# Kernel optimization log

Measured on AMD Instinct MI355X. Metric: run time of the kernel, lower is better.

The kernel has to match this reference:

```python
import jax, jax.numpy as jnp
import numpy as np

B, S, H, R = 32, 512, 1024, 64


def _bernoulli(key, shape, p=0.05):
    return (jax.random.uniform(key, shape) < p).astype(jnp.float32)


def setup_inputs() -> dict:
    key = jax.random.key(0)
    ks = jax.random.split(key, 16)
    context = jax.random.normal(ks[0], (B, S, H), dtype=jnp.float32)
    masks = jnp.ones((B, S), dtype=jnp.float32)
    all_subject_heads = _bernoulli(ks[1], (B, S))
    all_subject_tails = _bernoulli(ks[2], (B, S))
    # one-hot subject head/tail positions (tail >= head)
    h_pos = jax.random.randint(ks[3], (B,), 0, S // 2)
    t_pos = h_pos + jax.random.randint(ks[4], (B,), 0, 8)
    subject_head = jax.nn.one_hot(h_pos, S, dtype=jnp.float32)
    subject_tail = jax.nn.one_hot(t_pos, S, dtype=jnp.float32)
    object_heads = _bernoulli(ks[5], (B, S, R))
    object_tails = _bernoulli(ks[6], (B, S, R))
    # learned parameters (PyTorch Linear: y = x @ W.T + b; store as [in, out])
    sc = 1.0 / np.sqrt(H)
    Ws_h = jax.random.uniform(ks[7], (H, 1), minval=-sc, maxval=sc)
    bs_h = jnp.zeros((1,), dtype=jnp.float32)
    Ws_t = jax.random.uniform(ks[8], (H, 1), minval=-sc, maxval=sc)
    bs_t = jnp.zeros((1,), dtype=jnp.float32)
    Wo_h = jax.random.uniform(ks[9], (H, R), minval=-sc, maxval=sc)
    bo_h = jnp.zeros((R,), dtype=jnp.float32)
    Wo_t = jax.random.uniform(ks[10], (H, R), minval=-sc, maxval=sc)
    bo_t = jnp.zeros((R,), dtype=jnp.float32)
    return dict(context=context, masks=masks,
                all_subject_heads=all_subject_heads, all_subject_tails=all_subject_tails,
                subject_head=subject_head, subject_tail=subject_tail,
                object_heads=object_heads, object_tails=object_tails,
                Ws_h=Ws_h, bs_h=bs_h, Ws_t=Ws_t, bs_t=bs_t,
                Wo_h=Wo_h, bo_h=bo_h, Wo_t=Wo_t, bo_t=bo_t)


def _bce_with_logits(logits, targets):
    # numerically stable, matches F.binary_cross_entropy_with_logits(reduction='none')
    return jnp.maximum(logits, 0.0) - logits * targets + jnp.log1p(jnp.exp(-jnp.abs(logits)))


def _masked_loss(gold, pred, mask):
    loss = _bce_with_logits(pred, gold)
    if loss.ndim != mask.ndim:
        mask = mask[..., None]
    return jnp.sum(loss * mask) / jnp.sum(mask)


def reference(context, masks, all_subject_heads, all_subject_tails,
              subject_head, subject_tail, object_heads, object_tails,
              Ws_h, bs_h, Ws_t, bs_t, Wo_h, bo_h, Wo_t, bo_t):
    # subject logits: [B,S]
    pred_subject_heads = (context @ Ws_h + bs_h)[..., 0]
    pred_subject_tails = (context @ Ws_t + bs_t)[..., 0]
    # subject pooling: one-hot [B,S] x context [B,S,H] -> [B,H]
    sub_h = jnp.einsum('bs,bsh->bh', subject_head, context)
    sub_t = jnp.einsum('bs,bsh->bh', subject_tail, context)
    subject = (sub_h + sub_t) * 0.5
    context_subject = context + subject[:, None, :]  # [B,S,H]
    pred_object_heads = context_subject @ Wo_h + bo_h  # [B,S,R]
    pred_object_tails = context_subject @ Wo_t + bo_t  # [B,S,R]
    loss = (_masked_loss(all_subject_heads, pred_subject_heads, masks)
            + _masked_loss(all_subject_tails, pred_subject_tails, masks)
            + _masked_loss(object_heads, pred_object_heads, masks)
            + _masked_loss(object_tails, pred_object_tails, masks))
    return loss
```

## Files before the change

kernel.cpp:

```cpp
#include <hip/hip_runtime.h>


#define B_  32
#define S_  512
#define H_  1024
#define R_  64
#define M_  (B_ * S_)
#define NPAD 160
#define NVALID 130
#define NCOL 144
#define MT 64
#define PHK 512
#define TBLK 20

typedef __attribute__((ext_vector_type(4))) float  floatx4;
typedef __attribute__((ext_vector_type(8))) short  short8;
typedef __attribute__((ext_vector_type(8))) unsigned short u16x8;

__device__ __forceinline__ unsigned short f2bf(float f) {
    unsigned int u = __float_as_uint(f);
    u = (u + 0x7FFFu + ((u >> 16) & 1u)) >> 16;
    return (unsigned short)u;
}

__device__ __forceinline__ short8 cvt8(float4 a, float4 b) {
    union { unsigned short us[8]; short8 s8; } u;
    u.us[0] = f2bf(a.x); u.us[1] = f2bf(a.y); u.us[2] = f2bf(a.z); u.us[3] = f2bf(a.w);
    u.us[4] = f2bf(b.x); u.us[5] = f2bf(b.y); u.us[6] = f2bf(b.z); u.us[7] = f2bf(b.w);
    return u.s8;
}

__device__ __forceinline__ void gload16(const void* g, void* l) {
    __builtin_amdgcn_global_load_lds(
        (const __attribute__((address_space(1))) unsigned int*)g,
        (__attribute__((address_space(3))) unsigned int*)l, 16, 0, 0);
}

__global__ __launch_bounds__(256) void aux_kernel(
        const float* __restrict__ ctx, const float* __restrict__ head,
        const float* __restrict__ tail, const float* __restrict__ masks,
        const float* __restrict__ Wo_h, const float* __restrict__ Wo_t,
        const float* __restrict__ Ws_h, const float* __restrict__ Ws_t,
        const float* __restrict__ bo_h, const float* __restrict__ bo_t,
        const float* __restrict__ bs_h, const float* __restrict__ bs_t,
        unsigned short* __restrict__ WtG, float* __restrict__ rowBias,
        float* __restrict__ accum) {
    const int tid = threadIdx.x;
    __shared__ float tr[32][257];
    __shared__ float subj[H_];
    __shared__ float partS[4][256];
    __shared__ int cnt;
    __shared__ int   sidx[8];
    __shared__ float sw[8];

    if (blockIdx.x < TBLK) {
        const int kt = blockIdx.x / 5, nt = blockIdx.x % 5;
        const int k0 = kt * 256, n0 = nt * 32;
        if (n0 < 128) {
            const float* src = (n0 < 64) ? Wo_h : Wo_t;
            const int cb = n0 & 63;
            const int nn = tid & 31, kk = tid >> 5;
#pragma unroll
            for (int i = 0; i < 32; ++i) {
                const int k = k0 + i * 8 + kk;
                tr[nn][i * 8 + kk] = src[(size_t)k * R_ + cb + nn];
            }
            __syncthreads();
#pragma unroll
            for (int p = 0; p < 4; ++p) {
                const int chunk = p * 256 + tid;
                const int n = chunk >> 5;
                const int kc = (chunk & 31) * 8;
                u16x8 v;
#pragma unroll
                for (int j = 0; j < 8; ++j) v[j] = f2bf(tr[n][kc + j]);
                *(u16x8*)(WtG + (size_t)(n0 + n) * H_ + k0 + kc) = v;
            }
        } else {
#pragma unroll
            for (int p = 0; p < 4; ++p) {
                const int chunk = p * 256 + tid;
                const int n = 128 + (chunk >> 5);
                const int kc = (chunk & 31) * 8;
                u16x8 v;
#pragma unroll
                for (int j = 0; j < 8; ++j) {
                    float f = (n == 128) ? Ws_h[k0 + kc + j]
                            : (n == 129) ? Ws_t[k0 + kc + j] : 0.0f;
                    v[j] = f2bf(f);
                }
                *(u16x8*)(WtG + (size_t)n * H_ + k0 + kc) = v;
            }
        }
        return;
    }

    const int b = blockIdx.x - TBLK;
    if (tid == 0) cnt = 0;
    __syncthreads();
    float msk = 0.0f;
    for (int s = tid; s < S_; s += 256) {
        float w = 0.5f * (head[b * S_ + s] + tail[b * S_ + s]);
        if (w != 0.0f) {
            int i = atomicAdd(&cnt, 1);
            if (i < 8) { sidx[i] = s; sw[i] = w; }
        }
        msk += masks[b * S_ + s];
    }
    for (int o = 32; o > 0; o >>= 1) msk += __shfl_down(msk, o, 64);
    if ((tid & 63) == 0) atomicAdd(&accum[1], msk);
    __syncthreads();
    const int nnz = cnt < 8 ? cnt : 8;
    for (int h = tid; h < H_; h += 256) {
        float a = 0.0f;
        for (int i = 0; i < nnz; i++)
            a += sw[i] * ctx[((size_t)b * S_ + sidx[i]) * H_ + h];
        subj[h] = a;
    }
    __syncthreads();
    {
        const int cg = tid & 31;
        const int ks = tid >> 5;
        const int c4 = cg * 4;
        const float* W = (c4 < 64) ? Wo_h : Wo_t;
        const int cc = c4 & 63;
        const int kk0 = ks * 128;
        float ax = 0.f, ay = 0.f, az = 0.f, aw2 = 0.f;
#pragma unroll 4
        for (int k = kk0; k < kk0 + 128; ++k) {
            const float4 w = *(const float4*)(W + (size_t)k * R_ + cc);
            const float sv = subj[k];
            ax += sv * w.x; ay += sv * w.y; az += sv * w.z; aw2 += sv * w.w;
        }
        partS[0][tid] = ax; partS[1][tid] = ay;
        partS[2][tid] = az; partS[3][tid] = aw2;
    }
    __syncthreads();
    if (tid < NPAD) {
        float bias = tid < 64  ? bo_h[tid]
                   : tid < 128 ? bo_t[tid - 64]
                   : tid == 128 ? bs_h[0]
                   : tid == 129 ? bs_t[0] : 0.0f;
        float a2 = 0.0f;
        if (tid < 128) {
            const int g = tid >> 2, j = tid & 3;
#pragma unroll
            for (int s = 0; s < 8; ++s) a2 += partS[j][s * 32 + g];
        }
        rowBias[b * NPAD + tid] = bias + a2;
    }
}

__global__ __launch_bounds__(256, 1) void main_kernel(
        const float* __restrict__ ctx, const unsigned short* __restrict__ WtG,
        const float* __restrict__ rowBias, const float* __restrict__ masks,
        const float* __restrict__ ash, const float* __restrict__ ast,
        const float* __restrict__ oh, const float* __restrict__ ot,
        float* __restrict__ accum, float* __restrict__ out) {
    __shared__ __align__(16) unsigned short Bsm[NCOL * PHK];

    const int tid  = threadIdx.x;
    const int gm0  = blockIdx.x * MT;
    const int b    = gm0 >> 9;
    const int wave = tid >> 6, lane = tid & 63;
    const int lr = lane & 15, q = lane >> 4;

#define STAGE(kbase) do {                                                      \
        _Pragma("unroll")                                                      \
        for (int p = 0; p < (NCOL * PHK * 2 / 16) / 256; ++p) {        \
            const int i = p * 256 + tid;                                       \
            const int row = i >> 6;                                            \
            const int bcol = (i & 63) << 4;                                    \
            const int sb = bcol ^ ((row & 7) << 4);                            \
            gload16((const char*)(WtG + (size_t)row * H_ + (kbase)) + sb,      \
                    (char*)Bsm + (size_t)i * 16);                              \
        }                                                                      \
    } while (0)

    const float* aP = ctx + (size_t)(gm0 + wave * 16 + lr) * H_ + q * 8;
    const int swzr = (lr & 7) << 4;
    int rb9[9];
#pragma unroll
    for (int t = 0; t < 9; ++t) rb9[t] = (t * 16 + lr) * 1024;

    floatx4 acc[9];
#pragma unroll
    for (int t = 0; t < 9; ++t) acc[t] = (floatx4){0.f, 0.f, 0.f, 0.f};

#define COMPUTE(kbase) do {                                                    \
        _Pragma("unroll")                                                      \
        for (int ks = 0; ks < PHK / 32; ++ks) {                \
            const float4 f0 = *(const float4*)(aP + (kbase) + ks * 32);        \
            const float4 f1 = *(const float4*)(aP + (kbase) + ks * 32 + 4);    \
            const short8 afr = cvt8(f0, f1);                                   \
            const int kb = (ks * 64 + q * 16) ^ swzr;                          \
            _Pragma("unroll")                                                  \
            for (int t = 0; t < 9; ++t) {                                      \
                const short8 bfr = *(const short8*)((const char*)Bsm + rb9[t] + kb);\
                acc[t] = __builtin_amdgcn_mfma_f32_16x16x32_bf16(afr, bfr, acc[t], 0, 0, 0);\
            }                                                                  \
        }                                                                      \
    } while (0)

    STAGE(0);
    __syncthreads();
    COMPUTE(0);
    __syncthreads();
    STAGE(PHK);
    __syncthreads();
    COMPUTE(PHK);
#undef STAGE
#undef COMPUTE

    float lsum = 0.0f;
#pragma unroll
    for (int t = 0; t < 9; ++t) {
        const int col = t * 16 + lr;
        if (col < NVALID) {
            const float rbv = rowBias[b * NPAD + col];
#pragma unroll
            for (int i = 0; i < 4; ++i) {
                const int row = gm0 + wave * 16 + q * 4 + i;
                const float l = acc[t][i] + rbv;
                float tgt;
                if (col < 64)        tgt = oh[(size_t)row * R_ + col];
                else if (col < 128)  tgt = ot[(size_t)row * R_ + (col - 64)];
                else if (col == 128) tgt = ash[row];
                else                 tgt = ast[row];
                const float mk = masks[row];
                const float bce = fmaxf(l, 0.0f) - l * tgt + log1pf(__expf(-fabsf(l)));
                lsum += bce * mk;
            }
        }
    }
    for (int o = 32; o > 0; o >>= 1) lsum += __shfl_down(lsum, o, 64);
    if (lane == 0) {
        atomicAdd(&accum[0], lsum);
        __threadfence();
        const unsigned int prev = atomicAdd((unsigned int*)(accum + 2), 1u);
        if (prev == 4u * gridDim.x - 1u) {
            const float s = atomicAdd(&accum[0], 0.0f);
            const float m = atomicAdd(&accum[1], 0.0f);
            out[0] = s / m;
        }
    }
}

extern "C" void kernel_launch(void* const* d_in, const int* in_sizes, int n_in,
                              void* d_out, int out_size, void* d_ws, size_t ws_size,
                              hipStream_t stream) {
    const float* ctx   = (const float*)d_in[0];
    const float* masks = (const float*)d_in[1];
    const float* ash   = (const float*)d_in[2];
    const float* ast   = (const float*)d_in[3];
    const float* sh    = (const float*)d_in[4];
    const float* st    = (const float*)d_in[5];
    const float* oh    = (const float*)d_in[6];
    const float* ot    = (const float*)d_in[7];
    const float* Ws_h  = (const float*)d_in[8];
    const float* bs_h  = (const float*)d_in[9];
    const float* Ws_t  = (const float*)d_in[10];
    const float* bs_t  = (const float*)d_in[11];
    const float* Wo_h  = (const float*)d_in[12];
    const float* bo_h  = (const float*)d_in[13];
    const float* Wo_t  = (const float*)d_in[14];
    const float* bo_t  = (const float*)d_in[15];
    float* out = (float*)d_out;

    char* ws = (char*)d_ws;
    float* accum   = (float*)(ws + 0);
    float* rowBias = (float*)(ws + 256);
    unsigned short* WtG = (unsigned short*)(ws + 256 + 32 * NPAD * 4);

    hipMemsetAsync(accum, 0, 12, stream);
    aux_kernel<<<TBLK + B_, 256, 0, stream>>>(ctx, sh, st, masks, Wo_h, Wo_t,
                                              Ws_h, Ws_t, bo_h, bo_t, bs_h, bs_t,
                                              WtG, rowBias, accum);
    main_kernel<<<M_ / MT, 256, 0, stream>>>(ctx, WtG, rowBias, masks,
                                             ash, ast, oh, ot, accum, out);
}
```

Before: 197.5 us.

## Split K across four wave groups per block with LDS partial-sum reduction

The main kernel grows from 256 to 1024 threads per block. Each group of four waves handles one quarter of every staged K-phase for the same 64-row tile. The other three groups write their MFMA partial accumulators into the reused shared-memory buffer, and group zero sums them before running the BCE loss and the atomic reduction. The aim is more waves per CU, so the fp32 context loads and the MFMA latency are better hidden. The cost is an extra LDS round trip, more barriers, and a tighter per-thread register budget.

```diff
diff --git a/kernel.cpp b/kernel.cpp
--- a/kernel.cpp
+++ b/kernel.cpp
@@ -12,6 +12,7 @@
 #define MT 64
 #define PHK 512
 #define TBLK 20
+#define NTHR 1024
 
 typedef __attribute__((ext_vector_type(4))) float  floatx4;
 typedef __attribute__((ext_vector_type(8))) short  short8;
@@ -151,7 +152,7 @@
     }
 }
 
-__global__ __launch_bounds__(256, 1) void main_kernel(
+__global__ __launch_bounds__(NTHR, 4) void main_kernel(
         const float* __restrict__ ctx, const unsigned short* __restrict__ WtG,
         const float* __restrict__ rowBias, const float* __restrict__ masks,
         const float* __restrict__ ash, const float* __restrict__ ast,
@@ -163,13 +164,15 @@
     const int gm0  = blockIdx.x * MT;
     const int b    = gm0 >> 9;
     const int wave = tid >> 6, lane = tid & 63;
+    const int rg = wave & 3;
+    const int kq = wave >> 2;
     const int lr = lane & 15, q = lane >> 4;
 
 #define STAGE(kbase) do {                                                      \
         _Pragma("unroll")                                                      \
-        for (int p = 0; p < (NCOL * PHK * 2 / 16) / 256; ++p) {        \
-            const int i = p * 256 + tid;                                       \
-            const int row = i >> 6;                                            \
+        for (int p = 0; p < 9; ++p) {                                          \
+            const int i = p * NTHR + tid;                                      \
+            const int row = i >> 6;               \
             const int bcol = (i & 63) << 4;                                    \
             const int sb = bcol ^ ((row & 7) << 4);                            \
             gload16((const char*)(WtG + (size_t)row * H_ + (kbase)) + sb,      \
@@ -177,8 +180,8 @@
         }                                                                      \
     } while (0)
 
-    const float* aP = ctx + (size_t)(gm0 + wave * 16 + lr) * H_ + q * 8;
-    const int swzr = (lr & 7) << 4;
+    const float* aP = ctx + (size_t)(gm0 + rg * 16 + lr) * H_ + q * 8;
+    const int swz = (lr & 7) << 4;
     int rb9[9];
 #pragma unroll
     for (int t = 0; t < 9; ++t) rb9[t] = (t * 16 + lr) * 1024;
@@ -189,11 +192,12 @@
 
 #define COMPUTE(kbase) do {                                                    \
         _Pragma("unroll")                                                      \
-        for (int ks = 0; ks < PHK / 32; ++ks) {                \
-            const float4 f0 = *(const float4*)(aP + (kbase) + ks * 32);        \
-            const float4 f1 = *(const float4*)(aP + (kbase) + ks * 32 + 4);    \
+        for (int ks = 0; ks < 4; ++ks) {                                       \
+            const int kl = kq * 128 + ks * 32;                                 \
+            const float4 f0 = *(const float4*)(aP + (kbase) + kl);             \
+            const float4 f1 = *(const float4*)(aP + (kbase) + kl + 4);         \
             const short8 afr = cvt8(f0, f1);                                   \
-            const int kb = (ks * 64 + q * 16) ^ swzr;                          \
+            const int kb = (kl * 2 + q * 16) ^ swz;                            \
             _Pragma("unroll")                                                  \
             for (int t = 0; t < 9; ++t) {                                      \
                 const short8 bfr = *(const short8*)((const char*)Bsm + rb9[t] + kb);\
@@ -209,39 +213,62 @@
     STAGE(PHK);
     __syncthreads();
     COMPUTE(PHK);
+    __syncthreads();
 #undef STAGE
 #undef COMPUTE
 
-    float lsum = 0.0f;
-#pragma unroll
-    for (int t = 0; t < 9; ++t) {
-        const int col = t * 16 + lr;
-        if (col < NVALID) {
-            const float rbv = rowBias[b * NPAD + col];
+    float* Rf = (float*)Bsm;
+    if (kq > 0) {
+        const int base = ((kq - 1) * 4 + rg) * 2304;
+#pragma unroll
+        for (int t = 0; t < 9; ++t)
+#pragma unroll
+            for (int i = 0; i < 4; ++i)
+                Rf[base + (t * 4 + i) * 64 + lane] = acc[t][i];
+    }
+    __syncthreads();
+    if (kq == 0) {
+#pragma unroll
+        for (int t = 0; t < 9; ++t)
 #pragma unroll
             for (int i = 0; i < 4; ++i) {
-                const int row = gm0 + wave * 16 + q * 4 + i;
-                const float l = acc[t][i] + rbv;
-                float tgt;
-                if (col < 64)        tgt = oh[(size_t)row * R_ + col];
-                else if (col < 128)  tgt = ot[(size_t)row * R_ + (col - 64)];
-                else if (col == 128) tgt = ash[row];
-                else                 tgt = ast[row];
-                const float mk = masks[row];
-                const float bce = fmaxf(l, 0.0f) - l * tgt + log1pf(__expf(-fabsf(l)));
-                lsum += bce * mk;
-            }
-        }
-    }
-    for (int o = 32; o > 0; o >>= 1) lsum += __shfl_down(lsum, o, 64);
-    if (lane == 0) {
-        atomicAdd(&accum[0], lsum);
-        __threadfence();
-        const unsigned int prev = atomicAdd((unsigned int*)(accum + 2), 1u);
-        if (prev == 4u * gridDim.x - 1u) {
-            const float s = atomicAdd(&accum[0], 0.0f);
-            const float m = atomicAdd(&accum[1], 0.0f);
-            out[0] = s / m;
+                const int o = (t * 4 + i) * 64 + lane;
+                acc[t][i] = ((acc[t][i] + Rf[rg * 2304 + o])
+                             + Rf[(4 + rg) * 2304 + o])
+                             + Rf[(8 + rg) * 2304 + o];
+            }
+
+        float lsum = 0.0f;
+#pragma unroll
+        for (int t = 0; t < 9; ++t) {
+            const int col = t * 16 + lr;
+            if (col < NVALID) {
+                const float rbv = rowBias[b * NPAD + col];
+#pragma unroll
+                for (int i = 0; i < 4; ++i) {
+                    const int row = gm0 + rg * 16 + q * 4 + i;
+                    const float l = acc[t][i] + rbv;
+                    float tgt;
+                    if (col < 64)        tgt = oh[(size_t)row * R_ + col];
+                    else if (col < 128)  tgt = ot[(size_t)row * R_ + (col - 64)];
+                    else if (col == 128) tgt = ash[row];
+                    else                 tgt = ast[row];
+                    const float mk = masks[row];
+                    const float bce = fmaxf(l, 0.0f) - l * tgt + log1pf(__expf(-fabsf(l)));
+                    lsum += bce * mk;
+                }
+            }
+        }
+        for (int o = 32; o > 0; o >>= 1) lsum += __shfl_down(lsum, o, 64);
+        if (lane == 0) {
+            atomicAdd(&accum[0], lsum);
+            __threadfence();
+            const unsigned int prev = atomicAdd((unsigned int*)(accum + 2), 1u);
+            if (prev == 4u * gridDim.x - 1u) {
+                const float s = atomicAdd(&accum[0], 0.0f);
+                const float m = atomicAdd(&accum[1], 0.0f);
+                out[0] = s / m;
+            }
         }
     }
 }
@@ -276,6 +303,6 @@
     aux_kernel<<<TBLK + B_, 256, 0, stream>>>(ctx, sh, st, masks, Wo_h, Wo_t,
                                               Ws_h, Ws_t, bo_h, bo_t, bs_h, bs_t,
                                               WtG, rowBias, accum);
-    main_kernel<<<M_ / MT, 256, 0, stream>>>(ctx, WtG, rowBias, masks,
-                                             ash, ast, oh, ot, accum, out);
-}
+    main_kernel<<<M_ / MT, NTHR, 0, stream>>>(ctx, WtG, rowBias, masks,
+                                              ash, ast, oh, ot, accum, out);
+}
```

Result: faster. 178.7 us (-9.5%).
